# Kernel tuning notes

Hardware: AMD Instinct MI355X
Metric: run time of the kernel (lower is better)

The kernel has to match this reference:

```python
import jax, jax.numpy as jnp
import numpy as np
import math

B, S, F, H, C = 64, 64, 4096, 1024, 31


def setup_inputs() -> dict:
    key = jax.random.key(0)
    ks = jax.random.split(key, 10)
    inp = {
        "x": jax.random.normal(ks[0], (B, S, F), dtype=jnp.float32),
        "h0": jax.random.normal(ks[1], (B, H), dtype=jnp.float32),
        "Wxe": jax.random.normal(ks[2], (F, H), dtype=jnp.float32) / math.sqrt(F),
        "bxe": jnp.zeros((H,), jnp.float32),
        "Wep": jax.random.normal(ks[3], (H, C), dtype=jnp.float32) / math.sqrt(H),
        "bep": jnp.zeros((C,), jnp.float32),
        "Whr": jax.random.normal(ks[4], (H, H), dtype=jnp.float32) / math.sqrt(H),
        "bhr": jnp.zeros((H,), jnp.float32),
        "Wx0r": jax.random.normal(ks[5], (H, H), dtype=jnp.float32) / math.sqrt(H),
        "bx0r": jnp.zeros((H,), jnp.float32),
        "Wxtz": jax.random.normal(ks[6], (H, H), dtype=jnp.float32) / math.sqrt(H),
        "bxtz": jnp.zeros((H,), jnp.float32),
        "Wx0z": jax.random.normal(ks[7], (H, H), dtype=jnp.float32) / math.sqrt(H),
        "bx0z": jnp.zeros((H,), jnp.float32),
        "Wxth1": jax.random.normal(ks[8], (H, H), dtype=jnp.float32) / math.sqrt(H),
        "bxth1": jnp.zeros((H,), jnp.float32),
        "Wh1h1": jax.random.normal(ks[9], (H, H), dtype=jnp.float32) / math.sqrt(H),
        "bh1h1": jnp.zeros((H,), jnp.float32),
    }
    return inp


def reference(x, h0, Wxe, bxe, Wep, bep, Whr, bhr, Wx0r, bx0r,
              Wxtz, bxtz, Wx0z, bx0z, Wxth1, bxth1, Wh1h1, bh1h1):
    # x: (B, S, F); h0: (B, H)
    steps = x.shape[1]
    x0 = x[:, -1]                                            # current information

    # Input-dependent projections are independent of the recurrence -> batch them.
    xtes = jax.nn.relu(jnp.einsum('bsf,fh->bsh', x, Wxe) + bxe)   # (B,S,H)
    x0e = jax.nn.relu(x0 @ Wxe + bxe)                             # (B,H), constant over steps
    ptes = jnp.einsum('bsh,hc->bsc', xtes, Wep) + bep             # (B,S,C)
    p0e = x0e @ Wep + bep                                         # (B,C)

    x0r = x0e @ Wx0r + bx0r                                       # (B,H) step-invariant
    x0z = x0e @ Wx0z + bx0z
    xtz_all = jnp.einsum('bsh,hg->bsg', xtes, Wxtz) + bxtz        # (B,S,H)
    xth1_all = jnp.einsum('bsh,hg->bsg', xtes, Wxth1) + bxth1     # (B,S,H)

    def step(h, inputs):
        xtz, xth1 = inputs                                        # (B,H) each
        rt = jax.nn.sigmoid(h @ Whr + bhr + x0r)
        zt = jax.nn.sigmoid(xtz + x0z)
        h1_t_1 = h @ Wh1h1 + bh1h1
        ht1 = jnp.tanh(xth1 + rt * h1_t_1)
        ht = (1.0 - zt) * ht1 + zt * h
        return ht, ht

    # scan over time: move step axis to front
    xs = (jnp.swapaxes(xtz_all, 0, 1), jnp.swapaxes(xth1_all, 0, 1))  # (S,B,H)
    _, hts_t = jax.lax.scan(step, h0, xs)
    hts = jnp.swapaxes(hts_t, 0, 1)                               # (B,S,H)

    p0es = jnp.broadcast_to(p0e[:, None, :], (p0e.shape[0], steps, p0e.shape[1]))
    x0es = jnp.broadcast_to(x0e[:, None, :], (x0e.shape[0], steps, x0e.shape[1]))
    return (hts, ptes, p0es, x0es * 1.0, xtes) if False else (hts, ptes, p0es, xtes, x0es)
```

## Files before the change

kernel.cpp:

```cpp
#include <hip/hip_runtime.h>
#include <stdint.h>


using bf16 = __bf16;
typedef __attribute__((ext_vector_type(8))) __bf16 bf16x8;
typedef __attribute__((ext_vector_type(4))) float f32x4;

#define B_DIM 64
#define S_DIM 64
#define F_DIM 4096
#define H_DIM 1024
#define C_DIM 31


__global__ void cast_x_kernel(const float* __restrict__ in, bf16* __restrict__ out) {
  int i = blockIdx.x * 256 + threadIdx.x;
  const float4* p = (const float4*)in + (size_t)i * 2;
  float4 a = p[0], b = p[1];
  bf16x8 v;
  v[0] = (bf16)a.x; v[1] = (bf16)a.y; v[2] = (bf16)a.z; v[3] = (bf16)a.w;
  v[4] = (bf16)b.x; v[5] = (bf16)b.y; v[6] = (bf16)b.z; v[7] = (bf16)b.w;
  ((bf16x8*)out)[i] = v;
}

__global__ void tag_h0_kernel(const float* __restrict__ h0, unsigned* __restrict__ hT0) {
  int i = blockIdx.x * 256 + threadIdx.x;
  union { bf16 b; unsigned short u; } cv;
  cv.b = (bf16)h0[i];
  __hip_atomic_store(hT0 + i, ((unsigned)cv.u << 16), __ATOMIC_RELAXED,
                     __HIP_MEMORY_SCOPE_AGENT);
}

__global__ void transpose_cast(const float* __restrict__ in, bf16* __restrict__ out,
                               int R, int C) {
  __shared__ float t[64][65];
  int tR = blockIdx.x * 64, tC = blockIdx.y * 64;
  int tx = threadIdx.x & 63, ty = threadIdx.x >> 6;
#pragma unroll
  for (int i = 0; i < 16; ++i) {
    int r = tR + i * 4 + ty, c = tC + tx;
    t[i * 4 + ty][tx] = (r < R && c < C) ? in[(size_t)r * C + c] : 0.f;
  }
  __syncthreads();
#pragma unroll
  for (int i = 0; i < 16; ++i) {
    int c = tC + i * 4 + ty, r = tR + tx;
    if (c < C && r < R) out[(size_t)c * R + r] = (bf16)t[tx][i * 4 + ty];
  }
}

__global__ void transpose_cast_1k6(const float* __restrict__ a0, const float* __restrict__ a1,
                                   const float* __restrict__ a2, const float* __restrict__ a3,
                                   const float* __restrict__ a4, const float* __restrict__ a5,
                                   bf16* __restrict__ o0, bf16* __restrict__ o1,
                                   bf16* __restrict__ o2) {
  __shared__ float t[64][65];
  int z = blockIdx.z;
  const float* in = z == 0 ? a0 : z == 1 ? a1 : z == 2 ? a2 : z == 3 ? a3 : z == 4 ? a4 : a5;
  bf16* out = (z < 2 ? o0 : z < 4 ? o1 : o2) + (size_t)(z & 1) * 1048576;
  int tR = blockIdx.x * 64, tC = blockIdx.y * 64;
  int tx = threadIdx.x & 63, ty = threadIdx.x >> 6;
#pragma unroll
  for (int i = 0; i < 16; ++i)
    t[i * 4 + ty][tx] = in[(size_t)(tR + i * 4 + ty) * 1024 + tC + tx];
  __syncthreads();
#pragma unroll
  for (int i = 0; i < 16; ++i)
    out[(size_t)(tC + i * 4 + ty) * 1024 + tR + tx] = (bf16)t[tx][i * 4 + ty];
}

template <int MODE>
__launch_bounds__(256, 2)
__global__ void gemm_bt(const bf16* __restrict__ A, const bf16* __restrict__ B,
                        int M, int N, int K, int lda,
                        const float* __restrict__ bias0,
                        const float* __restrict__ bias1,
                        const float* __restrict__ bias2,
                        const float* __restrict__ x0rz,
                        float* __restrict__ outA,
                        float* __restrict__ outB,
                        float* __restrict__ outC,
                        bf16* __restrict__ outBf) {
  __shared__ bf16 ldsA[128 * 64];
  __shared__ bf16 ldsB[128 * 64];
  const int tid = threadIdx.x;
  const int lane = tid & 63;
  const int wave = tid >> 6;
  const int quad = lane >> 4;
  const int l15 = lane & 15;
  const int wm = wave & 1, wn = wave >> 1;
  const int m0 = blockIdx.x * 128, n0 = blockIdx.y * 128;

  f32x4 acc[4][4] = {};

  for (int kc = 0; kc < K; kc += 64) {
#pragma unroll
    for (int i = 0; i < 4; ++i) {
      int qb = i * 256 + wave * 64;
      int q = qb + lane;
      int r = q >> 3, cs = q & 7;
      int c = cs ^ (r & 7);
      int gr = m0 + r; if (gr > M - 1) gr = M - 1;
      __builtin_amdgcn_global_load_lds(
          (const __attribute__((address_space(1))) unsigned int*)(A + (size_t)gr * lda + kc + c * 8),
          (__attribute__((address_space(3))) unsigned int*)(ldsA + (size_t)qb * 8),
          16, 0, 0);
      __builtin_amdgcn_global_load_lds(
          (const __attribute__((address_space(1))) unsigned int*)(B + (size_t)(n0 + r) * K + kc + c * 8),
          (__attribute__((address_space(3))) unsigned int*)(ldsB + (size_t)qb * 8),
          16, 0, 0);
    }
    __syncthreads();
#pragma unroll
    for (int ks = 0; ks < 2; ++ks) {
      bf16x8 af[4], bfr[4];
      int ch = ks * 4 + quad;
#pragma unroll
      for (int t = 0; t < 4; ++t) {
        int ar = wm * 64 + t * 16 + l15;
        af[t] = *(const bf16x8*)(ldsA + ar * 64 + ((ch ^ (ar & 7)) * 8));
        int br = wn * 64 + t * 16 + l15;
        bfr[t] = *(const bf16x8*)(ldsB + br * 64 + ((ch ^ (br & 7)) * 8));
      }
#pragma unroll
      for (int mt = 0; mt < 4; ++mt)
#pragma unroll
        for (int nt = 0; nt < 4; ++nt)
          acc[mt][nt] = __builtin_amdgcn_mfma_f32_16x16x32_bf16(
              af[mt], bfr[nt], acc[mt][nt], 0, 0, 0);
    }
    __syncthreads();
  }

#pragma unroll
  for (int mt = 0; mt < 4; ++mt) {
#pragma unroll
    for (int nt = 0; nt < 4; ++nt) {
#pragma unroll
      for (int i = 0; i < 4; ++i) {
        int m = m0 + wm * 64 + mt * 16 + quad * 4 + i;
        int n = n0 + wn * 64 + nt * 16 + l15;
        if (m >= M) continue;
        float v = acc[mt][nt][i];
        if (MODE == 0) {
          v += bias0[n];
          v = fmaxf(v, 0.f);
          outA[(size_t)m * 1024 + n] = v;
          outBf[(size_t)m * 1024 + n] = (bf16)v;
        } else if (MODE == 1) {
          if (n < 1024) {
            float z = v + bias0[n] + x0rz[(size_t)(m >> 6) * 2048 + 1024 + n];
            outA[(size_t)m * 1024 + n] = 1.f / (1.f + expf(-z));
          } else if (n < 2048) {
            outB[(size_t)m * 1024 + (n - 1024)] = v + bias1[n - 1024];
          } else if (n < 2048 + C_DIM) {
            outC[(size_t)m * C_DIM + (n - 2048)] = v + bias2[n - 2048];
          }
        } else {
          outA[(size_t)m * 2048 + n] = v + (n < 1024 ? bias0[n] : bias1[n - 1024]);
        }
      }
    }
  }
}

#define TAG_OK(v, w) \
  ((((unsigned)(v) & 0xFFFFu) == (w)) & (((unsigned)((v) >> 32) & 0xFFFFu) == (w)))

__launch_bounds__(256, 1)
__global__ void recur_kernel(const bf16* __restrict__ WrecT,
                             const float* __restrict__ bhr,
                             const float* __restrict__ bh1h1,
                             const float* __restrict__ x0rz,
                             const float* __restrict__ ztAll,
                             const float* __restrict__ xth1All,
                             const float* __restrict__ h0,
                             unsigned* hT0,
                             unsigned* hT1,
                             float* __restrict__ hts) {
  __shared__ bf16 ldsA[16 * 1024];
  __shared__ float part[4][64][16];
  const int tid = threadIdx.x;
  const int lane = tid & 63, wave = tid >> 6;
  const int quad = lane >> 4, l15 = lane & 15;
  const int j = blockIdx.x >> 2;
  const int g = blockIdx.x & 3;
  const int kq = wave * 256;

  bf16x8 wr[2][8], wh[2][8];
#pragma unroll
  for (int tn = 0; tn < 2; ++tn) {
    int row = j * 32 + tn * 16 + l15;
#pragma unroll
    for (int kb = 0; kb < 8; ++kb) {
      wr[tn][kb] = *(const bf16x8*)(WrecT + (size_t)row * 1024 + kq + kb * 32 + quad * 8);
      wh[tn][kb] = *(const bf16x8*)(WrecT + (size_t)(1024 + row) * 1024 + kq + kb * 32 + quad * 8);
    }
  }

  float rb[2][4], hloc[2][4], hb2[2];
  if (wave == 0) {
#pragma unroll
    for (int tn = 0; tn < 2; ++tn) {
      int col = j * 32 + tn * 16 + l15;
      hb2[tn] = bh1h1[col];
#pragma unroll
      for (int i = 0; i < 4; ++i) {
        int b = g * 16 + quad * 4 + i;
        rb[tn][i] = bhr[col] + x0rz[(size_t)b * 2048 + col];
        hloc[tn][i] = h0[(size_t)b * 1024 + col];
      }
    }
  }

  for (int s = 0; s < 64; ++s) {
    const unsigned want = (unsigned)s;
    const unsigned* src = ((s & 1) ? hT1 : hT0) + (size_t)g * 16 * 1024;
    float zt[2][4], xh[2][4];
    if (wave == 0) {
#pragma unroll
      for (int tn = 0; tn < 2; ++tn)
#pragma unroll
        for (int i = 0; i < 4; ++i) {
          size_t mrow = ((size_t)(g * 16 + quad * 4 + i) * 64 + s) * 1024 + j * 32 + tn * 16 + l15;
          zt[tn][i] = ztAll[mrow];
          xh[tn][i] = xth1All[mrow];
        }
    }
    {
      int pend = (tid < 32) ? 1 : 0;
      const unsigned long long* sp =
          (const unsigned long long*)(src + (size_t)(tid & 15) * 1024 + (tid & 31) * 32);
      int iters = 0;
      while (true) {
        if (pend) {
          unsigned long long a = __hip_atomic_load(sp, __ATOMIC_RELAXED, __HIP_MEMORY_SCOPE_AGENT);
          unsigned long long b = __hip_atomic_load(sp + 1, __ATOMIC_RELAXED, __HIP_MEMORY_SCOPE_AGENT);
          if (TAG_OK(a, want) && TAG_OK(b, want)) pend = 0;
        }
        if (__syncthreads_count(pend) == 0) break;
        if (++iters > (1 << 16)) break;
        __builtin_amdgcn_s_sleep(1);
      }
    }
    const unsigned long long* s64 = (const unsigned long long*)src;
#pragma unroll
    for (int half = 0; half < 2; ++half) {
      unsigned long long q0[8], q1[8];
#pragma unroll
      for (int r8 = 0; r8 < 8; ++r8) {
        const unsigned long long* p = s64 + (size_t)(half * 8 + r8) * 512 + tid * 2;
        q0[r8] = __hip_atomic_load(p, __ATOMIC_RELAXED, __HIP_MEMORY_SCOPE_AGENT);
        q1[r8] = __hip_atomic_load(p + 1, __ATOMIC_RELAXED, __HIP_MEMORY_SCOPE_AGENT);
      }
      unsigned miss = 0;
#pragma unroll
      for (int r8 = 0; r8 < 8; ++r8)
        if (!(TAG_OK(q0[r8], want) && TAG_OK(q1[r8], want))) miss |= 1u << r8;
      for (int it = 0; miss && it < (1 << 14); ++it) {
#pragma unroll
        for (int r8 = 0; r8 < 8; ++r8)
          if (miss & (1u << r8)) {
            const unsigned long long* p = s64 + (size_t)(half * 8 + r8) * 512 + tid * 2;
            unsigned long long a = __hip_atomic_load(p, __ATOMIC_RELAXED, __HIP_MEMORY_SCOPE_AGENT);
            unsigned long long b = __hip_atomic_load(p + 1, __ATOMIC_RELAXED, __HIP_MEMORY_SCOPE_AGENT);
            if (TAG_OK(a, want) && TAG_OK(b, want)) {
              q0[r8] = a; q1[r8] = b;
              miss &= ~(1u << r8);
            }
          }
      }
#pragma unroll
      for (int r8 = 0; r8 < 8; ++r8) {
        int r = half * 8 + r8;
        unsigned d0 = (unsigned)q0[r8], d1 = (unsigned)(q0[r8] >> 32);
        unsigned d2 = (unsigned)q1[r8], d3 = (unsigned)(q1[r8] >> 32);
        unsigned long long pk =
            ((unsigned long long)((d2 >> 16) | (d3 & 0xFFFF0000u)) << 32) |
            ((d0 >> 16) | (d1 & 0xFFFF0000u));
        char* lp = (char*)ldsA + r * 2048 + (((tid >> 1) ^ (r & 7)) * 16) + (tid & 1) * 8;
        *(unsigned long long*)lp = pk;
      }
    }
    __syncthreads();
    f32x4 racc[2] = {}, hacc[2] = {};
#pragma unroll
    for (int kb = 0; kb < 8; ++kb) {
      int ch = wave * 32 + kb * 4 + quad;
      bf16x8 af = *(const bf16x8*)((char*)ldsA + l15 * 2048 + ((ch ^ (l15 & 7)) * 16));
      racc[0] = __builtin_amdgcn_mfma_f32_16x16x32_bf16(af, wr[0][kb], racc[0], 0, 0, 0);
      racc[1] = __builtin_amdgcn_mfma_f32_16x16x32_bf16(af, wr[1][kb], racc[1], 0, 0, 0);
      hacc[0] = __builtin_amdgcn_mfma_f32_16x16x32_bf16(af, wh[0][kb], hacc[0], 0, 0, 0);
      hacc[1] = __builtin_amdgcn_mfma_f32_16x16x32_bf16(af, wh[1][kb], hacc[1], 0, 0, 0);
    }
    *(f32x4*)&part[wave][lane][0]  = racc[0];
    *(f32x4*)&part[wave][lane][4]  = racc[1];
    *(f32x4*)&part[wave][lane][8]  = hacc[0];
    *(f32x4*)&part[wave][lane][12] = hacc[1];
    __syncthreads();
    if (wave == 0) {
#pragma unroll
      for (int w = 1; w < 4; ++w) {
        racc[0] += *(const f32x4*)&part[w][lane][0];
        racc[1] += *(const f32x4*)&part[w][lane][4];
        hacc[0] += *(const f32x4*)&part[w][lane][8];
        hacc[1] += *(const f32x4*)&part[w][lane][12];
      }
      unsigned* dst = (s & 1) ? hT0 : hT1;
#pragma unroll
      for (int tn = 0; tn < 2; ++tn)
#pragma unroll
        for (int i = 0; i < 4; ++i) {
          int b = g * 16 + quad * 4 + i;
          int col = j * 32 + tn * 16 + l15;
          size_t mrow = ((size_t)b * 64 + s) * 1024 + col;
          float rt = 1.f / (1.f + expf(-(racc[tn][i] + rb[tn][i])));
          float th = tanhf(xh[tn][i] + rt * (hacc[tn][i] + hb2[tn]));
          float hn = (1.f - zt[tn][i]) * th + zt[tn][i] * hloc[tn][i];
          hloc[tn][i] = hn;
          hts[mrow] = hn;
          if (s < 63) {
            union { bf16 b16; unsigned short u; } cv;
            cv.b16 = (bf16)hn;
            __hip_atomic_store(dst + (size_t)b * 1024 + col,
                               ((unsigned)cv.u << 16) | (unsigned)(s + 1),
                               __ATOMIC_RELAXED, __HIP_MEMORY_SCOPE_AGENT);
          }
        }
    }
  }
}

__global__ void bcast_x0es(const float* __restrict__ xtes, float* __restrict__ x0es) {
  int idx = blockIdx.x * 256 + threadIdx.x;
  int b = idx >> 14;
  int j = idx & 255;
  ((float4*)x0es)[idx] = ((const float4*)xtes)[(size_t)b * 16384 + 63 * 256 + j];
}

__global__ void bcast_p0es(const float* __restrict__ ptes, float* __restrict__ p0es) {
  int idx = blockIdx.x * 256 + threadIdx.x;
  if (idx >= B_DIM * S_DIM * C_DIM) return;
  int b = idx / (S_DIM * C_DIM);
  int rem = idx - b * (S_DIM * C_DIM);
  int c = rem % C_DIM;
  p0es[idx] = ptes[(size_t)b * (S_DIM * C_DIM) + 63 * C_DIM + c];
}

extern "C" void kernel_launch(void* const* d_in, const int* in_sizes, int n_in,
                              void* d_out, int out_size, void* d_ws, size_t ws_size,
                              hipStream_t stream) {
  const float* x     = (const float*)d_in[0];
  const float* h0    = (const float*)d_in[1];
  const float* Wxe   = (const float*)d_in[2];
  const float* bxe   = (const float*)d_in[3];
  const float* Wep   = (const float*)d_in[4];
  const float* bep   = (const float*)d_in[5];
  const float* Whr   = (const float*)d_in[6];
  const float* bhr   = (const float*)d_in[7];
  const float* Wx0r  = (const float*)d_in[8];
  const float* bx0r  = (const float*)d_in[9];
  const float* Wxtz  = (const float*)d_in[10];
  const float* bxtz  = (const float*)d_in[11];
  const float* Wx0z  = (const float*)d_in[12];
  const float* bx0z  = (const float*)d_in[13];
  const float* Wxth1 = (const float*)d_in[14];
  const float* bxth1 = (const float*)d_in[15];
  const float* Wh1h1 = (const float*)d_in[16];
  const float* bh1h1 = (const float*)d_in[17];

  float* out   = (float*)d_out;
  float* hts   = out;
  float* ptes  = out + 4194304;
  float* p0es  = out + 4321280;
  float* xtesO = out + 4448256;
  float* x0es  = out + 8642560;

  char* ws = (char*)d_ws;
  size_t off = 0;
  auto alloc = [&](size_t bytes) -> char* {
    char* p = ws + off;
    off += (bytes + 255) & ~(size_t)255;
    return p;
  };
  bf16*  xbf     = (bf16*)alloc(33554432);
  float* ztAll   = (float*)xbf;
  float* xth1All = (float*)((char*)xbf + 16777216);
  bf16*  WxeT    = (bf16*)alloc(8388608);
  bf16*  W2T     = (bf16*)alloc((size_t)2176 * 1024 * 2);
  bf16*  WrecT   = (bf16*)alloc(4194304);
  bf16*  Wx0T    = (bf16*)alloc(4194304);
  bf16*  xtesBf  = (bf16*)alloc(8388608);
  float* x0rz    = (float*)alloc(524288);
  unsigned* hT0  = (unsigned*)alloc(262144);
  unsigned* hT1  = (unsigned*)alloc(262144);

  hipMemsetAsync(W2T, 0, (size_t)2176 * 1024 * 2, stream);

  cast_x_kernel<<<8192, 256, 0, stream>>>(x, xbf);
  tag_h0_kernel<<<256, 256, 0, stream>>>(h0, hT0);

  dim3 tb(256);
  transpose_cast<<<dim3(64, 16), tb, 0, stream>>>(Wxe, WxeT, 4096, 1024);
  transpose_cast_1k6<<<dim3(16, 16, 6), tb, 0, stream>>>(
      Whr, Wh1h1, Wxtz, Wxth1, Wx0r, Wx0z, WrecT, W2T, Wx0T);
  transpose_cast<<<dim3(16, 1), tb, 0, stream>>>(Wep, W2T + 2048 * 1024, 1024, 31);

  gemm_bt<0><<<dim3(32, 8), tb, 0, stream>>>(xbf, WxeT, 4096, 1024, 4096, 4096,
                                             bxe, nullptr, nullptr, nullptr,
                                             xtesO, nullptr, nullptr, xtesBf);
  gemm_bt<2><<<dim3(1, 16), tb, 0, stream>>>(xtesBf + 63 * 1024, Wx0T, 64, 2048, 1024, 65536,
                                             bx0r, bx0z, nullptr, nullptr,
                                             x0rz, nullptr, nullptr, nullptr);
  gemm_bt<1><<<dim3(32, 17), tb, 0, stream>>>(xtesBf, W2T, 4096, 2176, 1024, 1024,
                                              bxtz, bxth1, bep, x0rz,
                                              ztAll, xth1All, ptes, nullptr);

  recur_kernel<<<128, tb, 0, stream>>>(WrecT, bhr, bh1h1, x0rz, ztAll, xth1All,
                                       h0, hT0, hT1, hts);

  bcast_x0es<<<4096, tb, 0, stream>>>(xtesO, x0es);
  bcast_p0es<<<496, tb, 0, stream>>>(ptes, p0es);
}
```

Measured before the change: 666.1 us.

## Fuse prep kernels, split-K x0 GEMM, fold broadcasts into GEMMs, restructure recurrence

Merges the x cast and h0 tagging into one launch and all weight transposes into another. The x0 projection GEMM now uses split-K with atomic accumulation into a zeroed buffer. The x0es and p0es broadcasts are written from the GEMM epilogues instead of separate kernels. The recurrence kernel drops to 64 blocks, each wave owning 16 columns over the full K, which removes the cross-wave LDS reduction and the pre-poll barrier. The cost is more register pressure, fewer CUs in the serial loop, and atomics in the x0 GEMM.

```diff
diff --git a/kernel.cpp b/kernel.cpp
--- a/kernel.cpp
+++ b/kernel.cpp
@@ -12,29 +12,29 @@
 #define H_DIM 1024
 #define C_DIM 31
 
-
-__global__ void cast_x_kernel(const float* __restrict__ in, bf16* __restrict__ out) {
-  int i = blockIdx.x * 256 + threadIdx.x;
-  const float4* p = (const float4*)in + (size_t)i * 2;
-  float4 a = p[0], b = p[1];
-  bf16x8 v;
-  v[0] = (bf16)a.x; v[1] = (bf16)a.y; v[2] = (bf16)a.z; v[3] = (bf16)a.w;
-  v[4] = (bf16)b.x; v[5] = (bf16)b.y; v[6] = (bf16)b.z; v[7] = (bf16)b.w;
-  ((bf16x8*)out)[i] = v;
-}
-
-__global__ void tag_h0_kernel(const float* __restrict__ h0, unsigned* __restrict__ hT0) {
-  int i = blockIdx.x * 256 + threadIdx.x;
-  union { bf16 b; unsigned short u; } cv;
-  cv.b = (bf16)h0[i];
-  __hip_atomic_store(hT0 + i, ((unsigned)cv.u << 16), __ATOMIC_RELAXED,
-                     __HIP_MEMORY_SCOPE_AGENT);
-}
-
-__global__ void transpose_cast(const float* __restrict__ in, bf16* __restrict__ out,
-                               int R, int C) {
+__global__ void cast_tag_kernel(const float* __restrict__ x, bf16* __restrict__ xbf,
+                                const float* __restrict__ h0, unsigned* __restrict__ hT0) {
+  int bx = blockIdx.x;
+  if (bx < 8192) {
+    int i = bx * 256 + threadIdx.x;
+    const float4* p = (const float4*)x + (size_t)i * 2;
+    float4 a = p[0], b = p[1];
+    bf16x8 v;
+    v[0] = (bf16)a.x; v[1] = (bf16)a.y; v[2] = (bf16)a.z; v[3] = (bf16)a.w;
+    v[4] = (bf16)b.x; v[5] = (bf16)b.y; v[6] = (bf16)b.z; v[7] = (bf16)b.w;
+    ((bf16x8*)xbf)[i] = v;
+  } else {
+    int i = (bx - 8192) * 256 + threadIdx.x;
+    union { bf16 b; unsigned short u; } cv;
+    cv.b = (bf16)h0[i];
+    __hip_atomic_store(hT0 + i, ((unsigned)cv.u << 16), __ATOMIC_RELAXED,
+                       __HIP_MEMORY_SCOPE_AGENT);
+  }
+}
+
+__device__ __forceinline__ void tr64(const float* __restrict__ in, bf16* __restrict__ out,
+                                     int R, int C, int tR, int tC) {
   __shared__ float t[64][65];
-  int tR = blockIdx.x * 64, tC = blockIdx.y * 64;
   int tx = threadIdx.x & 63, ty = threadIdx.x >> 6;
 #pragma unroll
   for (int i = 0; i < 16; ++i) {
@@ -49,24 +49,24 @@
   }
 }
 
-__global__ void transpose_cast_1k6(const float* __restrict__ a0, const float* __restrict__ a1,
-                                   const float* __restrict__ a2, const float* __restrict__ a3,
-                                   const float* __restrict__ a4, const float* __restrict__ a5,
-                                   bf16* __restrict__ o0, bf16* __restrict__ o1,
-                                   bf16* __restrict__ o2) {
-  __shared__ float t[64][65];
-  int z = blockIdx.z;
-  const float* in = z == 0 ? a0 : z == 1 ? a1 : z == 2 ? a2 : z == 3 ? a3 : z == 4 ? a4 : a5;
-  bf16* out = (z < 2 ? o0 : z < 4 ? o1 : o2) + (size_t)(z & 1) * 1048576;
-  int tR = blockIdx.x * 64, tC = blockIdx.y * 64;
-  int tx = threadIdx.x & 63, ty = threadIdx.x >> 6;
-#pragma unroll
-  for (int i = 0; i < 16; ++i)
-    t[i * 4 + ty][tx] = in[(size_t)(tR + i * 4 + ty) * 1024 + tC + tx];
-  __syncthreads();
-#pragma unroll
-  for (int i = 0; i < 16; ++i)
-    out[(size_t)(tC + i * 4 + ty) * 1024 + tR + tx] = (bf16)t[tx][i * 4 + ty];
+__global__ void transpose_all(const float* __restrict__ Wxe, bf16* __restrict__ WxeT,
+                              const float* __restrict__ a0, const float* __restrict__ a1,
+                              const float* __restrict__ a2, const float* __restrict__ a3,
+                              const float* __restrict__ a4, const float* __restrict__ a5,
+                              bf16* __restrict__ o0, bf16* __restrict__ o1,
+                              bf16* __restrict__ o2,
+                              const float* __restrict__ Wep, bf16* __restrict__ WepT) {
+  int id = blockIdx.x;
+  if (id < 1024) {
+    tr64(Wxe, WxeT, 4096, 1024, (id & 63) * 64, (id >> 6) * 64);
+  } else if (id < 2560) {
+    int q = id - 1024, z = q >> 8, t = q & 255;
+    const float* in = z == 0 ? a0 : z == 1 ? a1 : z == 2 ? a2 : z == 3 ? a3 : z == 4 ? a4 : a5;
+    bf16* out = (z < 2 ? o0 : z < 4 ? o1 : o2) + (size_t)(z & 1) * 1048576;
+    tr64(in, out, 1024, 1024, (t & 15) * 64, (t >> 4) * 64);
+  } else {
+    tr64(Wep, WepT, 1024, 31, (id - 2560) * 64, 0);
+  }
 }
 
 template <int MODE>
@@ -80,6 +80,7 @@
                         float* __restrict__ outA,
                         float* __restrict__ outB,
                         float* __restrict__ outC,
+                        float* __restrict__ outD,
                         bf16* __restrict__ outBf) {
   __shared__ bf16 ldsA[128 * 64];
   __shared__ bf16 ldsB[128 * 64];
@@ -90,10 +91,12 @@
   const int l15 = lane & 15;
   const int wm = wave & 1, wn = wave >> 1;
   const int m0 = blockIdx.x * 128, n0 = blockIdx.y * 128;
+  const int kPer = K / gridDim.z;
+  const int k0 = blockIdx.z * kPer;
 
   f32x4 acc[4][4] = {};
 
-  for (int kc = 0; kc < K; kc += 64) {
+  for (int kc = k0; kc < k0 + kPer; kc += 64) {
 #pragma unroll
     for (int i = 0; i < 4; ++i) {
       int qb = i * 256 + wave * 64;
@@ -147,6 +150,10 @@
           v = fmaxf(v, 0.f);
           outA[(size_t)m * 1024 + n] = v;
           outBf[(size_t)m * 1024 + n] = (bf16)v;
+          if ((m & 63) == 63) {
+            size_t base = (size_t)(m >> 6) * 64 * 1024 + n;
+            for (int sp = 0; sp < 64; ++sp) outD[base + (size_t)sp * 1024] = v;
+          }
         } else if (MODE == 1) {
           if (n < 1024) {
             float z = v + bias0[n] + x0rz[(size_t)(m >> 6) * 2048 + 1024 + n];
@@ -154,10 +161,16 @@
           } else if (n < 2048) {
             outB[(size_t)m * 1024 + (n - 1024)] = v + bias1[n - 1024];
           } else if (n < 2048 + C_DIM) {
-            outC[(size_t)m * C_DIM + (n - 2048)] = v + bias2[n - 2048];
+            float pv = v + bias2[n - 2048];
+            outC[(size_t)m * C_DIM + (n - 2048)] = pv;
+            if ((m & 63) == 63) {
+              size_t base = (size_t)(m >> 6) * 64 * C_DIM + (n - 2048);
+              for (int sp = 0; sp < 64; ++sp) outD[base + (size_t)sp * C_DIM] = pv;
+            }
           }
         } else {
-          outA[(size_t)m * 2048 + n] = v + (n < 1024 ? bias0[n] : bias1[n - 1024]);
+          if (k0 == 0) v += (n < 1024 ? bias0[n] : bias1[n - 1024]);
+          atomicAdd(outA + (size_t)m * 2048 + n, v);
         }
       }
     }
@@ -178,78 +191,47 @@
                              unsigned* hT0,
                              unsigned* hT1,
                              float* __restrict__ hts) {
-  __shared__ bf16 ldsA[16 * 1024];
-  __shared__ float part[4][64][16];
+  __shared__ bf16 ldsA[2][16 * 1024];
   const int tid = threadIdx.x;
   const int lane = tid & 63, wave = tid >> 6;
   const int quad = lane >> 4, l15 = lane & 15;
   const int j = blockIdx.x >> 2;
   const int g = blockIdx.x & 3;
-  const int kq = wave * 256;
-
-  bf16x8 wr[2][8], wh[2][8];
-#pragma unroll
-  for (int tn = 0; tn < 2; ++tn) {
-    int row = j * 32 + tn * 16 + l15;
-#pragma unroll
-    for (int kb = 0; kb < 8; ++kb) {
-      wr[tn][kb] = *(const bf16x8*)(WrecT + (size_t)row * 1024 + kq + kb * 32 + quad * 8);
-      wh[tn][kb] = *(const bf16x8*)(WrecT + (size_t)(1024 + row) * 1024 + kq + kb * 32 + quad * 8);
-    }
-  }
-
-  float rb[2][4], hloc[2][4], hb2[2];
-  if (wave == 0) {
-#pragma unroll
-    for (int tn = 0; tn < 2; ++tn) {
-      int col = j * 32 + tn * 16 + l15;
-      hb2[tn] = bh1h1[col];
-#pragma unroll
-      for (int i = 0; i < 4; ++i) {
-        int b = g * 16 + quad * 4 + i;
-        rb[tn][i] = bhr[col] + x0rz[(size_t)b * 2048 + col];
-        hloc[tn][i] = h0[(size_t)b * 1024 + col];
-      }
-    }
+  const int col = j * 64 + wave * 16 + l15;
+
+  bf16x8 wr[32], wh[32];
+#pragma unroll
+  for (int kb = 0; kb < 32; ++kb) {
+    wr[kb] = *(const bf16x8*)(WrecT + (size_t)col * 1024 + kb * 32 + quad * 8);
+    wh[kb] = *(const bf16x8*)(WrecT + (size_t)(1024 + col) * 1024 + kb * 32 + quad * 8);
+  }
+  float hb_ = bh1h1[col];
+  float rb[4], hloc[4];
+#pragma unroll
+  for (int i = 0; i < 4; ++i) {
+    int b = g * 16 + quad * 4 + i;
+    rb[i] = bhr[col] + x0rz[(size_t)b * 2048 + col];
+    hloc[i] = h0[(size_t)b * 1024 + col];
   }
 
   for (int s = 0; s < 64; ++s) {
     const unsigned want = (unsigned)s;
-    const unsigned* src = ((s & 1) ? hT1 : hT0) + (size_t)g * 16 * 1024;
-    float zt[2][4], xh[2][4];
-    if (wave == 0) {
-#pragma unroll
-      for (int tn = 0; tn < 2; ++tn)
-#pragma unroll
-        for (int i = 0; i < 4; ++i) {
-          size_t mrow = ((size_t)(g * 16 + quad * 4 + i) * 64 + s) * 1024 + j * 32 + tn * 16 + l15;
-          zt[tn][i] = ztAll[mrow];
-          xh[tn][i] = xth1All[mrow];
-        }
-    }
-    {
-      int pend = (tid < 32) ? 1 : 0;
-      const unsigned long long* sp =
-          (const unsigned long long*)(src + (size_t)(tid & 15) * 1024 + (tid & 31) * 32);
-      int iters = 0;
-      while (true) {
-        if (pend) {
-          unsigned long long a = __hip_atomic_load(sp, __ATOMIC_RELAXED, __HIP_MEMORY_SCOPE_AGENT);
-          unsigned long long b = __hip_atomic_load(sp + 1, __ATOMIC_RELAXED, __HIP_MEMORY_SCOPE_AGENT);
-          if (TAG_OK(a, want) && TAG_OK(b, want)) pend = 0;
-        }
-        if (__syncthreads_count(pend) == 0) break;
-        if (++iters > (1 << 16)) break;
-        __builtin_amdgcn_s_sleep(1);
-      }
-    }
-    const unsigned long long* s64 = (const unsigned long long*)src;
+    const unsigned long long* src =
+        (const unsigned long long*)(((s & 1) ? hT1 : hT0) + (size_t)g * 16384);
+    float zt[4], xh[4];
+#pragma unroll
+    for (int i = 0; i < 4; ++i) {
+      size_t mrow = ((size_t)(g * 16 + quad * 4 + i) * 64 + s) * 1024 + col;
+      zt[i] = ztAll[mrow];
+      xh[i] = xth1All[mrow];
+    }
+    bf16* dstL = ldsA[s & 1];
 #pragma unroll
     for (int half = 0; half < 2; ++half) {
       unsigned long long q0[8], q1[8];
 #pragma unroll
       for (int r8 = 0; r8 < 8; ++r8) {
-        const unsigned long long* p = s64 + (size_t)(half * 8 + r8) * 512 + tid * 2;
+        const unsigned long long* p = src + (size_t)(half * 8 + r8) * 512 + tid * 2;
         q0[r8] = __hip_atomic_load(p, __ATOMIC_RELAXED, __HIP_MEMORY_SCOPE_AGENT);
         q1[r8] = __hip_atomic_load(p + 1, __ATOMIC_RELAXED, __HIP_MEMORY_SCOPE_AGENT);
       }
@@ -257,11 +239,11 @@
 #pragma unroll
       for (int r8 = 0; r8 < 8; ++r8)
         if (!(TAG_OK(q0[r8], want) && TAG_OK(q1[r8], want))) miss |= 1u << r8;
-      for (int it = 0; miss && it < (1 << 14); ++it) {
+      for (int it = 0; miss && it < (1 << 20); ++it) {
 #pragma unroll
         for (int r8 = 0; r8 < 8; ++r8)
           if (miss & (1u << r8)) {
-            const unsigned long long* p = s64 + (size_t)(half * 8 + r8) * 512 + tid * 2;
+            const unsigned long long* p = src + (size_t)(half * 8 + r8) * 512 + tid * 2;
             unsigned long long a = __hip_atomic_load(p, __ATOMIC_RELAXED, __HIP_MEMORY_SCOPE_AGENT);
             unsigned long long b = __hip_atomic_load(p + 1, __ATOMIC_RELAXED, __HIP_MEMORY_SCOPE_AGENT);
             if (TAG_OK(a, want) && TAG_OK(b, want)) {
@@ -278,73 +260,39 @@
         unsigned long long pk =
             ((unsigned long long)((d2 >> 16) | (d3 & 0xFFFF0000u)) << 32) |
             ((d0 >> 16) | (d1 & 0xFFFF0000u));
-        char* lp = (char*)ldsA + r * 2048 + (((tid >> 1) ^ (r & 7)) * 16) + (tid & 1) * 8;
-        *(unsigned long long*)lp = pk;
+        int cc = ((tid >> 1) & 0x78) | (((tid >> 1) ^ r) & 7);
+        *(unsigned long long*)((char*)dstL + r * 2048 + cc * 16 + (tid & 1) * 8) = pk;
       }
     }
     __syncthreads();
-    f32x4 racc[2] = {}, hacc[2] = {};
-#pragma unroll
-    for (int kb = 0; kb < 8; ++kb) {
-      int ch = wave * 32 + kb * 4 + quad;
-      bf16x8 af = *(const bf16x8*)((char*)ldsA + l15 * 2048 + ((ch ^ (l15 & 7)) * 16));
-      racc[0] = __builtin_amdgcn_mfma_f32_16x16x32_bf16(af, wr[0][kb], racc[0], 0, 0, 0);
-      racc[1] = __builtin_amdgcn_mfma_f32_16x16x32_bf16(af, wr[1][kb], racc[1], 0, 0, 0);
-      hacc[0] = __builtin_amdgcn_mfma_f32_16x16x32_bf16(af, wh[0][kb], hacc[0], 0, 0, 0);
-      hacc[1] = __builtin_amdgcn_mfma_f32_16x16x32_bf16(af, wh[1][kb], hacc[1], 0, 0, 0);
-    }
-    *(f32x4*)&part[wave][lane][0]  = racc[0];
-    *(f32x4*)&part[wave][lane][4]  = racc[1];
-    *(f32x4*)&part[wave][lane][8]  = hacc[0];
-    *(f32x4*)&part[wave][lane][12] = hacc[1];
-    __syncthreads();
-    if (wave == 0) {
-#pragma unroll
-      for (int w = 1; w < 4; ++w) {
-        racc[0] += *(const f32x4*)&part[w][lane][0];
-        racc[1] += *(const f32x4*)&part[w][lane][4];
-        hacc[0] += *(const f32x4*)&part[w][lane][8];
-        hacc[1] += *(const f32x4*)&part[w][lane][12];
-      }
-      unsigned* dst = (s & 1) ? hT0 : hT1;
-#pragma unroll
-      for (int tn = 0; tn < 2; ++tn)
-#pragma unroll
-        for (int i = 0; i < 4; ++i) {
-          int b = g * 16 + quad * 4 + i;
-          int col = j * 32 + tn * 16 + l15;
-          size_t mrow = ((size_t)b * 64 + s) * 1024 + col;
-          float rt = 1.f / (1.f + expf(-(racc[tn][i] + rb[tn][i])));
-          float th = tanhf(xh[tn][i] + rt * (hacc[tn][i] + hb2[tn]));
-          float hn = (1.f - zt[tn][i]) * th + zt[tn][i] * hloc[tn][i];
-          hloc[tn][i] = hn;
-          hts[mrow] = hn;
-          if (s < 63) {
-            union { bf16 b16; unsigned short u; } cv;
-            cv.b16 = (bf16)hn;
-            __hip_atomic_store(dst + (size_t)b * 1024 + col,
-                               ((unsigned)cv.u << 16) | (unsigned)(s + 1),
-                               __ATOMIC_RELAXED, __HIP_MEMORY_SCOPE_AGENT);
-          }
-        }
-    }
-  }
-}
-
-__global__ void bcast_x0es(const float* __restrict__ xtes, float* __restrict__ x0es) {
-  int idx = blockIdx.x * 256 + threadIdx.x;
-  int b = idx >> 14;
-  int j = idx & 255;
-  ((float4*)x0es)[idx] = ((const float4*)xtes)[(size_t)b * 16384 + 63 * 256 + j];
-}
-
-__global__ void bcast_p0es(const float* __restrict__ ptes, float* __restrict__ p0es) {
-  int idx = blockIdx.x * 256 + threadIdx.x;
-  if (idx >= B_DIM * S_DIM * C_DIM) return;
-  int b = idx / (S_DIM * C_DIM);
-  int rem = idx - b * (S_DIM * C_DIM);
-  int c = rem % C_DIM;
-  p0es[idx] = ptes[(size_t)b * (S_DIM * C_DIM) + 63 * C_DIM + c];
+    f32x4 racc = {0.f, 0.f, 0.f, 0.f}, hacc = {0.f, 0.f, 0.f, 0.f};
+#pragma unroll
+    for (int kb = 0; kb < 32; ++kb) {
+      int ch = kb * 4 + quad;
+      bf16x8 af = *(const bf16x8*)((char*)dstL + l15 * 2048 +
+                                   (((ch & 0x78) | ((ch ^ l15) & 7)) * 16));
+      racc = __builtin_amdgcn_mfma_f32_16x16x32_bf16(af, wr[kb], racc, 0, 0, 0);
+      hacc = __builtin_amdgcn_mfma_f32_16x16x32_bf16(af, wh[kb], hacc, 0, 0, 0);
+    }
+    unsigned* dst = (s & 1) ? hT0 : hT1;
+#pragma unroll
+    for (int i = 0; i < 4; ++i) {
+      int b = g * 16 + quad * 4 + i;
+      size_t mrow = ((size_t)b * 64 + s) * 1024 + col;
+      float rt = 1.f / (1.f + expf(-(racc[i] + rb[i])));
+      float th = tanhf(xh[i] + rt * (hacc[i] + hb_));
+      float hn = (1.f - zt[i]) * th + zt[i] * hloc[i];
+      hloc[i] = hn;
+      hts[mrow] = hn;
+      if (s < 63) {
+        union { bf16 b16; unsigned short u; } cv;
+        cv.b16 = (bf16)hn;
+        __hip_atomic_store(dst + (size_t)b * 1024 + col,
+                           ((unsigned)cv.u << 16) | (unsigned)(s + 1),
+                           __ATOMIC_RELAXED, __HIP_MEMORY_SCOPE_AGENT);
+      }
+    }
+  }
 }
 
 extern "C" void kernel_launch(void* const* d_in, const int* in_sizes, int n_in,
@@ -396,29 +344,25 @@
   unsigned* hT1  = (unsigned*)alloc(262144);
 
   hipMemsetAsync(W2T, 0, (size_t)2176 * 1024 * 2, stream);
-
-  cast_x_kernel<<<8192, 256, 0, stream>>>(x, xbf);
-  tag_h0_kernel<<<256, 256, 0, stream>>>(h0, hT0);
+  hipMemsetAsync(x0rz, 0, 524288, stream);
 
   dim3 tb(256);
-  transpose_cast<<<dim3(64, 16), tb, 0, stream>>>(Wxe, WxeT, 4096, 1024);
-  transpose_cast_1k6<<<dim3(16, 16, 6), tb, 0, stream>>>(
-      Whr, Wh1h1, Wxtz, Wxth1, Wx0r, Wx0z, WrecT, W2T, Wx0T);
-  transpose_cast<<<dim3(16, 1), tb, 0, stream>>>(Wep, W2T + 2048 * 1024, 1024, 31);
+  cast_tag_kernel<<<8448, tb, 0, stream>>>(x, xbf, h0, hT0);
+  transpose_all<<<2576, tb, 0, stream>>>(Wxe, WxeT,
+                                         Whr, Wh1h1, Wxtz, Wxth1, Wx0r, Wx0z,
+                                         WrecT, W2T, Wx0T,
+                                         Wep, W2T + 2048 * 1024);
 
   gemm_bt<0><<<dim3(32, 8), tb, 0, stream>>>(xbf, WxeT, 4096, 1024, 4096, 4096,
                                              bxe, nullptr, nullptr, nullptr,
-                                             xtesO, nullptr, nullptr, xtesBf);
-  gemm_bt<2><<<dim3(1, 16), tb, 0, stream>>>(xtesBf + 63 * 1024, Wx0T, 64, 2048, 1024, 65536,
-                                             bx0r, bx0z, nullptr, nullptr,
-                                             x0rz, nullptr, nullptr, nullptr);
+                                             xtesO, nullptr, nullptr, x0es, xtesBf);
+  gemm_bt<2><<<dim3(1, 16, 4), tb, 0, stream>>>(xtesBf + 63 * 1024, Wx0T, 64, 2048, 1024, 65536,
+                                                bx0r, bx0z, nullptr, nullptr,
+                                                x0rz, nullptr, nullptr, nullptr, nullptr);
   gemm_bt<1><<<dim3(32, 17), tb, 0, stream>>>(xtesBf, W2T, 4096, 2176, 1024, 1024,
                                               bxtz, bxth1, bep, x0rz,
-                                              ztAll, xth1All, ptes, nullptr);
-
-  recur_kernel<<<128, tb, 0, stream>>>(WrecT, bhr, bh1h1, x0rz, ztAll, xth1All,
-                                       h0, hT0, hT1, hts);
-
-  bcast_x0es<<<4096, tb, 0, stream>>>(xtesO, x0es);
-  bcast_p0es<<<496, tb, 0, stream>>>(ptes, p0es);
-}
+                                              ztAll, xth1All, ptes, p0es, nullptr);
+
+  recur_kernel<<<64, tb, 0, stream>>>(WrecT, bhr, bh1h1, x0rz, ztAll, xth1All,
+                                      h0, hT0, hT1, hts);
+}
```

Result: faster. 605.8 us (-9.0%).
